# Performance work log

Measured on AMD Instinct MI355X. Metric: run time of the kernel, lower is better.

## Reference

```python
import jax, jax.numpy as jnp
import numpy as np

BATCH = 4096
DIM = 256
TEMPERATURE = 0.5
EPS = 1e-8  # torch CosineSimilarity norm clamp


def setup_inputs() -> dict:
    key = jax.random.key(0)
    k1, k2 = jax.random.split(key)
    zA = jax.random.normal(k1, (BATCH, DIM), dtype=jnp.float32)
    zB = jax.random.normal(k2, (BATCH, DIM), dtype=jnp.float32)
    return {"zA": zA, "zB": zB}


def reference(zA, zB):
    b = zA.shape[0]
    N = 2 * b
    z = jnp.concatenate([zA, zB], axis=0)                      # [N, D]
    norm = jnp.maximum(jnp.linalg.norm(z, axis=1, keepdims=True), EPS)
    zn = z / norm
    # cosine-similarity matrix via normalize + GEMM (same math as the
    # broadcasted CosineSimilarity(dim=2) in the original)
    sim = (zn @ zn.T) / TEMPERATURE                            # [N, N]

    idx = jnp.arange(N)
    pos = sim[idx, (idx + b) % N]                              # diag(+b) ++ diag(-b)

    # CE with label 0 over logits=[pos, negatives]; the logit set per row is
    # exactly {all j != i} (pos partner included once), so mask only the diagonal.
    neg_inf = jnp.finfo(sim.dtype).min
    masked = jnp.where(jnp.eye(N, dtype=bool), neg_inf, sim)
    per_row = jax.nn.logsumexp(masked, axis=1) - pos           # [N]
    loss = jnp.sum(per_row) / N                                # reduction='sum' / N
    return loss
```

## Files before the change

kernel.cpp:

```cpp
#include <hip/hip_runtime.h>
#include <hip/hip_bf16.h>

#define N_ROWS 8192
#define BATCH 4096
#define DIM 256
#define INV_T 2.0f

#define MTILE 128
#define CCHUNK 1024
#define NCHUNK 8
#define CT 16
#define LDSROW 528
#define LDSBUF (CT * LDSROW)

typedef __attribute__((ext_vector_type(8))) short bfrag8;
typedef __attribute__((ext_vector_type(4))) float facc4;

__global__ __launch_bounds__(256) void normalize_kernel(
    const float* __restrict__ zA, const float* __restrict__ zB,
    __hip_bfloat16* __restrict__ zn) {
    int tid = threadIdx.x;
    int wave = tid >> 6, lane = tid & 63;
    int row = blockIdx.x * 4 + wave;
    const float* src = (row < BATCH) ? (zA + (size_t)row * DIM)
                                     : (zB + (size_t)(row - BATCH) * DIM);
    float4 v = ((const float4*)src)[lane];
    float ss = v.x * v.x + v.y * v.y + v.z * v.z + v.w * v.w;
    #pragma unroll
    for (int m = 32; m; m >>= 1) ss += __shfl_xor(ss, m);
    float inv = 1.0f / fmaxf(sqrtf(ss), 1e-8f);
    union { ushort4 u; __hip_bfloat16 h[4]; } o;
    o.h[0] = __float2bfloat16(v.x * inv);
    o.h[1] = __float2bfloat16(v.y * inv);
    o.h[2] = __float2bfloat16(v.z * inv);
    o.h[3] = __float2bfloat16(v.w * inv);
    ((ushort4*)zn)[(size_t)row * (DIM / 4) + lane] = o.u;
}

__global__ __launch_bounds__(256, 2) void ntxent_main(
    const __hip_bfloat16* __restrict__ zn_,
    float* __restrict__ ep, float* __restrict__ pp) {
    const char* zn = (const char*)zn_;
    __shared__ char lds[2 * LDSBUF] __attribute__((aligned(16)));
    int tid = threadIdx.x, lane = tid & 63, wave = tid >> 6;
    int quad = lane >> 4, l15 = lane & 15;
    int row0 = blockIdx.x * MTILE + wave * 32;
    int chunk = blockIdx.y;
    int cc = chunk * CCHUNK;

    bfrag8 a[2][8];
    #pragma unroll
    for (int s = 0; s < 2; s++) {
        const char* ap = zn + (size_t)(row0 + s * 16 + l15) * 512 + quad * 16;
        #pragma unroll
        for (int ks = 0; ks < 8; ks++)
            a[s][ks] = *(const bfrag8*)(ap + ks * 64);
    }

    float es[2][4] = {{0.f,0.f,0.f,0.f},{0.f,0.f,0.f,0.f}};
    float ps[2][4] = {{0.f,0.f,0.f,0.f},{0.f,0.f,0.f,0.f}};

    int col0 = tid >> 5, j0 = tid & 31;
    unsigned lofs0 = col0 * LDSROW + j0 * 16;
    unsigned lofs1 = (col0 + 8) * LDSROW + j0 * 16;
    unsigned gofs0 = col0 * 512 + j0 * 16;
    unsigned gofs1 = (col0 + 8) * 512 + j0 * 16;
    const char* gbase = zn + (size_t)cc * 512;

    {
        uint4 r0 = *(const uint4*)(gbase + gofs0);
        uint4 r1 = *(const uint4*)(gbase + gofs1);
        *(uint4*)(lds + lofs0) = r0;
        *(uint4*)(lds + lofs1) = r1;
    }
    __syncthreads();

    const int NT = CCHUNK / CT;
    for (int t = 0; t < NT; t++) {
        char* cur = lds + (t & 1) * LDSBUF;
        char* nxt = lds + ((t + 1) & 1) * LDSBUF;
        uint4 s0, s1;
        if (t + 1 < NT) {
            const char* g = gbase + (size_t)(t + 1) * CT * 512;
            s0 = *(const uint4*)(g + gofs0);
            s1 = *(const uint4*)(g + gofs1);
        }
        const char* bp = cur + l15 * LDSROW + quad * 16;
        facc4 acc0 = {0.f, 0.f, 0.f, 0.f}, acc1 = {0.f, 0.f, 0.f, 0.f};
        #pragma unroll
        for (int ks = 0; ks < 8; ks++) {
            bfrag8 bf = *(const bfrag8*)(bp + ks * 64);
            acc0 = __builtin_amdgcn_mfma_f32_16x16x32_bf16(a[0][ks], bf, acc0, 0, 0, 0);
            acc1 = __builtin_amdgcn_mfma_f32_16x16x32_bf16(a[1][ks], bf, acc1, 0, 0, 0);
        }
        int gcol = cc + t * CT + l15;
        #pragma unroll
        for (int r = 0; r < 4; r++) {
            int grow = row0 + quad * 4 + r;
            float sim = acc0[r] * INV_T;
            float e = __expf(sim);
            if (gcol == grow) e = 0.0f;
            es[0][r] += e;
            if (gcol == (grow ^ BATCH)) ps[0][r] += sim;
        }
        #pragma unroll
        for (int r = 0; r < 4; r++) {
            int grow = row0 + 16 + quad * 4 + r;
            float sim = acc1[r] * INV_T;
            float e = __expf(sim);
            if (gcol == grow) e = 0.0f;
            es[1][r] += e;
            if (gcol == (grow ^ BATCH)) ps[1][r] += sim;
        }
        if (t + 1 < NT) {
            *(uint4*)(nxt + lofs0) = s0;
            *(uint4*)(nxt + lofs1) = s1;
        }
        __syncthreads();
    }

    #pragma unroll
    for (int s = 0; s < 2; s++)
        #pragma unroll
        for (int r = 0; r < 4; r++) {
            float e = es[s][r], p = ps[s][r];
            #pragma unroll
            for (int m = 1; m < 16; m <<= 1) {
                e += __shfl_xor(e, m);
                p += __shfl_xor(p, m);
            }
            if (l15 == 0) {
                int grow = row0 + s * 16 + quad * 4 + r;
                ep[(size_t)chunk * N_ROWS + grow] = e;
                pp[(size_t)chunk * N_ROWS + grow] = p;
            }
        }
}

__global__ __launch_bounds__(256) void finalize_kernel(
    const float* __restrict__ ep, const float* __restrict__ pp,
    float* __restrict__ out) {
    int tid = threadIdx.x;
    float acc = 0.0f;
    for (int i = tid; i < N_ROWS; i += 256) {
        float e = 0.0f, p = 0.0f;
        #pragma unroll
        for (int c = 0; c < NCHUNK; c++) {
            e += ep[(size_t)c * N_ROWS + i];
            p += pp[(size_t)c * N_ROWS + i];
        }
        acc += __logf(e) - p;
    }
    #pragma unroll
    for (int m = 32; m; m >>= 1) acc += __shfl_xor(acc, m);
    __shared__ float wsum[4];
    if ((tid & 63) == 0) wsum[tid >> 6] = acc;
    __syncthreads();
    if (tid == 0)
        out[0] = (wsum[0] + wsum[1] + wsum[2] + wsum[3]) * (1.0f / N_ROWS);
}

extern "C" void kernel_launch(void* const* d_in, const int* in_sizes, int n_in,
                              void* d_out, int out_size, void* d_ws, size_t ws_size,
                              hipStream_t stream) {
    const float* zA = (const float*)d_in[0];
    const float* zB = (const float*)d_in[1];
    float* out = (float*)d_out;
    char* ws = (char*)d_ws;
    __hip_bfloat16* zn = (__hip_bfloat16*)ws;
    float* ep = (float*)(ws + (size_t)N_ROWS * DIM * 2);
    float* pp = ep + (size_t)NCHUNK * N_ROWS;

    normalize_kernel<<<N_ROWS / 4, 256, 0, stream>>>(zA, zB, zn);
    dim3 grid(N_ROWS / MTILE, NCHUNK);
    ntxent_main<<<grid, 256, 0, stream>>>(zn, ep, pp);
    finalize_kernel<<<1, 256, 0, stream>>>(ep, pp, out);
}
```

Measured before the change: 122.6 us.

## Enlarge row tile per wave, specialize diagonal/positive tiles, parallelize finalize

Each wave now covers 64 rows instead of 32 (MTILE 256, CCHUNK 512), so every LDS B-fragment load feeds four MFMAs instead of two. This raises arithmetic intensity but also register pressure. Diagonal and positive-pair masking is now applied only on the tiles that can hold them, and exp is computed as exp2 with a prescaled constant. The positive logit is written once per row, and finalize runs across 32 blocks with an atomicAdd after a memset instead of a single block.

```diff
diff --git a/kernel.cpp b/kernel.cpp
--- a/kernel.cpp
+++ b/kernel.cpp
@@ -4,14 +4,14 @@
 #define N_ROWS 8192
 #define BATCH 4096
 #define DIM 256
-#define INV_T 2.0f
 
-#define MTILE 128
-#define CCHUNK 1024
-#define NCHUNK 8
+#define MTILE 256
+#define CCHUNK 512
+#define NCHUNK 16
 #define CT 16
 #define LDSROW 528
 #define LDSBUF (CT * LDSROW)
+#define KEXP 2.8853900817779268f
 
 typedef __attribute__((ext_vector_type(8))) short bfrag8;
 typedef __attribute__((ext_vector_type(4))) float facc4;
@@ -44,21 +44,24 @@
     __shared__ char lds[2 * LDSBUF] __attribute__((aligned(16)));
     int tid = threadIdx.x, lane = tid & 63, wave = tid >> 6;
     int quad = lane >> 4, l15 = lane & 15;
-    int row0 = blockIdx.x * MTILE + wave * 32;
+    int row0 = blockIdx.x * MTILE + wave * 64;
     int chunk = blockIdx.y;
     int cc = chunk * CCHUNK;
 
-    bfrag8 a[2][8];
+    bfrag8 a[4][8];
     #pragma unroll
-    for (int s = 0; s < 2; s++) {
+    for (int s = 0; s < 4; s++) {
         const char* ap = zn + (size_t)(row0 + s * 16 + l15) * 512 + quad * 16;
         #pragma unroll
         for (int ks = 0; ks < 8; ks++)
             a[s][ks] = *(const bfrag8*)(ap + ks * 64);
     }
 
-    float es[2][4] = {{0.f,0.f,0.f,0.f},{0.f,0.f,0.f,0.f}};
-    float ps[2][4] = {{0.f,0.f,0.f,0.f},{0.f,0.f,0.f,0.f}};
+    float es[4][4], ps[4][4];
+    #pragma unroll
+    for (int s = 0; s < 4; s++)
+        #pragma unroll
+        for (int r = 0; r < 4; r++) { es[s][r] = 0.f; ps[s][r] = 0.f; }
 
     int col0 = tid >> 5, j0 = tid & 31;
     unsigned lofs0 = col0 * LDSROW + j0 * 16;
@@ -86,32 +89,52 @@
             s1 = *(const uint4*)(g + gofs1);
         }
         const char* bp = cur + l15 * LDSROW + quad * 16;
-        facc4 acc0 = {0.f, 0.f, 0.f, 0.f}, acc1 = {0.f, 0.f, 0.f, 0.f};
+        bfrag8 bf[8];
         #pragma unroll
-        for (int ks = 0; ks < 8; ks++) {
-            bfrag8 bf = *(const bfrag8*)(bp + ks * 64);
-            acc0 = __builtin_amdgcn_mfma_f32_16x16x32_bf16(a[0][ks], bf, acc0, 0, 0, 0);
-            acc1 = __builtin_amdgcn_mfma_f32_16x16x32_bf16(a[1][ks], bf, acc1, 0, 0, 0);
+        for (int ks = 0; ks < 8; ks++)
+            bf[ks] = *(const bfrag8*)(bp + ks * 64);
+
+        facc4 acc[4];
+        #pragma unroll
+        for (int s = 0; s < 4; s++) acc[s] = (facc4){0.f, 0.f, 0.f, 0.f};
+        #pragma unroll
+        for (int ks = 0; ks < 8; ks++)
+            #pragma unroll
+            for (int s = 0; s < 4; s++)
+                acc[s] = __builtin_amdgcn_mfma_f32_16x16x32_bf16(a[s][ks], bf[ks], acc[s], 0, 0, 0);
+
+        int ctile = cc + t * CT;
+        int gcol = ctile + l15;
+        bool isdiag = (ctile >> 6) == (row0 >> 6);
+        bool ispos  = (ctile >> 6) == ((row0 ^ BATCH) >> 6);
+        if (isdiag) {
+            #pragma unroll
+            for (int s = 0; s < 4; s++)
+                #pragma unroll
+                for (int r = 0; r < 4; r++) {
+                    int grow = row0 + s * 16 + quad * 4 + r;
+                    float e = __builtin_amdgcn_exp2f(acc[s][r] * KEXP);
+                    if (gcol == grow) e = 0.0f;
+                    es[s][r] += e;
+                }
+        } else if (ispos) {
+            #pragma unroll
+            for (int s = 0; s < 4; s++)
+                #pragma unroll
+                for (int r = 0; r < 4; r++) {
+                    int grow = row0 + s * 16 + quad * 4 + r;
+                    float d = acc[s][r];
+                    es[s][r] += __builtin_amdgcn_exp2f(d * KEXP);
+                    if (gcol == (grow ^ BATCH)) ps[s][r] += d;
+                }
+        } else {
+            #pragma unroll
+            for (int s = 0; s < 4; s++)
+                #pragma unroll
+                for (int r = 0; r < 4; r++)
+                    es[s][r] += __builtin_amdgcn_exp2f(acc[s][r] * KEXP);
         }
-        int gcol = cc + t * CT + l15;
-        #pragma unroll
-        for (int r = 0; r < 4; r++) {
-            int grow = row0 + quad * 4 + r;
-            float sim = acc0[r] * INV_T;
-            float e = __expf(sim);
-            if (gcol == grow) e = 0.0f;
-            es[0][r] += e;
-            if (gcol == (grow ^ BATCH)) ps[0][r] += sim;
-        }
-        #pragma unroll
-        for (int r = 0; r < 4; r++) {
-            int grow = row0 + 16 + quad * 4 + r;
-            float sim = acc1[r] * INV_T;
-            float e = __expf(sim);
-            if (gcol == grow) e = 0.0f;
-            es[1][r] += e;
-            if (gcol == (grow ^ BATCH)) ps[1][r] += sim;
-        }
+
         if (t + 1 < NT) {
             *(uint4*)(nxt + lofs0) = s0;
             *(uint4*)(nxt + lofs1) = s1;
@@ -119,8 +142,9 @@
         __syncthreads();
     }
 
+    bool poswave = (((row0 ^ BATCH) >> 9) == chunk);
     #pragma unroll
-    for (int s = 0; s < 2; s++)
+    for (int s = 0; s < 4; s++)
         #pragma unroll
         for (int r = 0; r < 4; r++) {
             float e = es[s][r], p = ps[s][r];
@@ -132,7 +156,7 @@
             if (l15 == 0) {
                 int grow = row0 + s * 16 + quad * 4 + r;
                 ep[(size_t)chunk * N_ROWS + grow] = e;
-                pp[(size_t)chunk * N_ROWS + grow] = p;
+                if (poswave) pp[grow] = p;
             }
         }
 }
@@ -141,23 +165,18 @@
     const float* __restrict__ ep, const float* __restrict__ pp,
     float* __restrict__ out) {
     int tid = threadIdx.x;
-    float acc = 0.0f;
-    for (int i = tid; i < N_ROWS; i += 256) {
-        float e = 0.0f, p = 0.0f;
-        #pragma unroll
-        for (int c = 0; c < NCHUNK; c++) {
-            e += ep[(size_t)c * N_ROWS + i];
-            p += pp[(size_t)c * N_ROWS + i];
-        }
-        acc += __logf(e) - p;
-    }
+    int i = blockIdx.x * 256 + tid;
+    float e = 0.0f;
     #pragma unroll
-    for (int m = 32; m; m >>= 1) acc += __shfl_xor(acc, m);
+    for (int c = 0; c < NCHUNK; c++) e += ep[(size_t)c * N_ROWS + i];
+    float v = __logf(e) - 2.0f * pp[i];
+    #pragma unroll
+    for (int m = 32; m; m >>= 1) v += __shfl_xor(v, m);
     __shared__ float wsum[4];
-    if ((tid & 63) == 0) wsum[tid >> 6] = acc;
+    if ((tid & 63) == 0) wsum[tid >> 6] = v;
     __syncthreads();
     if (tid == 0)
-        out[0] = (wsum[0] + wsum[1] + wsum[2] + wsum[3]) * (1.0f / N_ROWS);
+        atomicAdd(out, (wsum[0] + wsum[1] + wsum[2] + wsum[3]) * (1.0f / N_ROWS));
 }
 
 extern "C" void kernel_launch(void* const* d_in, const int* in_sizes, int n_in,
@@ -171,8 +190,9 @@
     float* ep = (float*)(ws + (size_t)N_ROWS * DIM * 2);
     float* pp = ep + (size_t)NCHUNK * N_ROWS;
 
+    hipMemsetAsync(out, 0, sizeof(float), stream);
     normalize_kernel<<<N_ROWS / 4, 256, 0, stream>>>(zA, zB, zn);
     dim3 grid(N_ROWS / MTILE, NCHUNK);
     ntxent_main<<<grid, 256, 0, stream>>>(zn, ep, pp);
-    finalize_kernel<<<1, 256, 0, stream>>>(ep, pp, out);
+    finalize_kernel<<<N_ROWS / 256, 256, 0, stream>>>(ep, pp, out);
 }
```

Result: faster. 104.1 us (-15.1%).
